# Kernel tuning notes

Measured on AMD Instinct MI355X. Metric: run time of the kernel, lower is better.

The kernel has to match this reference:

```python
import jax, jax.numpy as jnp
import numpy as np

TAU = 0.3
NEG_SLOPE = 0.2
COS_EPS = 1e-8


def _masked_softmax(logits, mask, axis):
    # mask: bool, True = participates. Rows with no True entries yield zeros.
    neg = jnp.finfo(logits.dtype).min
    x = jnp.where(mask, logits, neg)
    x = x - jnp.max(x, axis=axis, keepdims=True)
    e = jnp.exp(x) * mask
    return e / jnp.maximum(jnp.sum(e, axis=axis, keepdims=True), 1e-16)


def _gat_layer(h, adj, W, a_src, a_dst, w_edge, a_edge, b):
    # Dense masked GATConv (heads=1). adj[b,i,j]=True means edge src j -> dst i.
    g = jnp.einsum('bld,dc->blc', h, W)            # projected features
    al_s = jnp.einsum('blc,c->bl', g, a_src)        # per-node src score
    al_d = jnp.einsum('blc,c->bl', g, a_dst)        # per-node dst score
    # edge_attr is constant 1.0 for every thresholded edge, so the edge term
    # lin_edge(1.0) . att_edge collapses to a scalar.
    ae = jnp.dot(w_edge, a_edge)
    logits = jax.nn.leaky_relu(al_d[:, :, None] + al_s[:, None, :] + ae, NEG_SLOPE)
    attn = _masked_softmax(logits, adj, axis=-1)    # softmax over incoming edges per dst
    out = jnp.einsum('bij,bjc->bic', attn, g) + b
    return jax.nn.relu(out)


def setup_inputs() -> dict:
    key = jax.random.key(0)
    B, L, D, H = 16, 1024, 768, 128
    ks = jax.random.split(key, 20)
    inp = {}
    inp['hidden'] = jax.random.normal(ks[0], (B, L, D), jnp.float32)
    inp['attention_mask'] = jax.random.randint(ks[1], (B, L), 0, 2, jnp.int32)

    def lin(k, i, o):
        return jax.random.normal(k, (i, o), jnp.float32) * (1.0 / np.sqrt(i))

    dims = [D, H]
    for l in range(2):
        i = dims[l]
        inp[f'W{l}'] = lin(ks[2 + 6 * l], i, H)
        inp[f'att_src{l}'] = jax.random.normal(ks[3 + 6 * l], (H,), jnp.float32) * 0.1
        inp[f'att_dst{l}'] = jax.random.normal(ks[4 + 6 * l], (H,), jnp.float32) * 0.1
        inp[f'w_edge{l}'] = jax.random.normal(ks[5 + 6 * l], (H,), jnp.float32) * 0.1
        inp[f'att_edge{l}'] = jax.random.normal(ks[6 + 6 * l], (H,), jnp.float32) * 0.1
        inp[f'bias{l}'] = jnp.zeros((H,), jnp.float32)
    out_dim = D + 2 * H            # jk_mode='cat' -> 1024
    hid = max(128, out_dim // 2)   # 512
    inp['S1_W'] = lin(ks[14], out_dim, hid)
    inp['S1_b'] = jnp.zeros((hid,), jnp.float32)
    inp['S2_W'] = lin(ks[15], hid, 1)
    inp['S2_b'] = jnp.zeros((1,), jnp.float32)
    return inp


def reference(hidden, attention_mask,
              W0, att_src0, att_dst0, w_edge0, att_edge0, bias0,
              W1, att_src1, att_dst1, w_edge1, att_edge1, bias1,
              S1_W, S1_b, S2_W, S2_b):
    valid = attention_mask.astype(bool)                         # (B,L)
    # per-batch pairwise cosine similarity graph, thresholded at TAU
    nrm = jnp.linalg.norm(hidden, axis=-1, keepdims=True)
    hn = hidden / jnp.maximum(nrm, COS_EPS)
    sim = jnp.einsum('bld,bmd->blm', hn, hn)                    # (B,L,L)
    adj = (sim > TAU) & valid[:, :, None] & valid[:, None, :]   # bool mask; diag (self loops) kept, sim=1>tau

    h1 = _gat_layer(hidden, adj, W0, att_src0, att_dst0, w_edge0, att_edge0, bias0)
    h2 = _gat_layer(h1, adj, W1, att_src1, att_dst1, w_edge1, att_edge1, bias1)
    h_all = jnp.concatenate([hidden, h1, h2], axis=-1)          # jk 'cat': (B,L,D+2H)

    scores = (jnp.tanh(h_all @ S1_W + S1_b) @ S2_W + S2_b)[..., 0]  # (B,L)
    weights = _masked_softmax(scores, valid, axis=-1)           # segment softmax per batch element
    pooled = jnp.einsum('bl,bld->bd', weights, h_all)           # segment scatter_add pooling
    return pooled
```

## Files before the change

### kernel.cpp

```cpp
#include <hip/hip_runtime.h>

typedef __attribute__((ext_vector_type(8))) short short8;
typedef __attribute__((ext_vector_type(4))) short s4v;
typedef __attribute__((ext_vector_type(4))) float f32x4;
typedef unsigned short u16;
typedef unsigned int u32;
typedef unsigned long long u64;

#define TAU_F 0.3f

__device__ __forceinline__ u16 f2bf(float f){
  u32 u = __float_as_uint(f);
  u32 r = u + 0x7FFFu + ((u >> 16) & 1u);
  return (u16)(r >> 16);
}
__device__ __forceinline__ float bf2f(u16 v){
  return __uint_as_float(((u32)v) << 16);
}
__device__ __forceinline__ float tanh_fast(float x){
  const float e = __expf(2.f * x);
  return 1.f - 2.f / (e + 1.f);
}

typedef __attribute__((address_space(1))) const u32 glb_u32;
typedef __attribute__((address_space(3))) u32 lds_u32;
__device__ __forceinline__ void async_lds16(const void* g, void* l){
  __builtin_amdgcn_global_load_lds((glb_u32*)g, (lds_u32*)l, 16, 0, 0);
}

__global__ __launch_bounds__(1024)
void pre_kernel(float* __restrict__ out, float* __restrict__ scores,
                const float* __restrict__ W0, u16* __restrict__ w0t,
                const float* __restrict__ W1, u16* __restrict__ w1t,
                const float* __restrict__ S1W, u16* __restrict__ s1t,
                const float* __restrict__ wed0, const float* __restrict__ aed0,
                const float* __restrict__ wed1, const float* __restrict__ aed1,
                float* __restrict__ aeb,
                const float* __restrict__ asrc0, const float* __restrict__ adst0,
                const float* __restrict__ asrc1, const float* __restrict__ adst1,
                float* __restrict__ u0, float* __restrict__ v0,
                float* __restrict__ u1, float* __restrict__ v1,
                const int* __restrict__ mask, int* __restrict__ cnt, int* __restrict__ idxb)
{
  __shared__ float lds[64*65];
  const int blk = blockIdx.x, t = threadIdx.x;

  auto tr_tile = [&](const float* in, u16* o, int K, int N, int kt, int ntile) {
    const int r = t >> 4, c0 = (t & 15) * 4;
    const int k0 = kt*64, n0 = ntile*64;
    const float4 v = *(const float4*)&in[(long)(k0 + r)*N + n0 + c0];
    lds[r*65 + c0 + 0] = v.x; lds[r*65 + c0 + 1] = v.y;
    lds[r*65 + c0 + 2] = v.z; lds[r*65 + c0 + 3] = v.w;
    __syncthreads();
    const u64 pk = (u64)f2bf(lds[(c0+0)*65 + r])
                 | ((u64)f2bf(lds[(c0+1)*65 + r]) << 16)
                 | ((u64)f2bf(lds[(c0+2)*65 + r]) << 32)
                 | ((u64)f2bf(lds[(c0+3)*65 + r]) << 48);
    *(u64*)&o[(long)(n0 + r)*K + k0 + c0] = pk;
  };

  if (blk < 16)  { out[blk*1024 + t] = 0.f; return; }
  if (blk < 32)  { scores[(blk-16)*1024 + t] = 0.f; return; }
  if (blk < 56)  { const int id = blk-32;  tr_tile(W0,  w0t, 768, 128, id >> 1, id & 1); return; }
  if (blk < 60)  { const int id = blk-56;  tr_tile(W1,  w1t, 128, 128, id >> 1, id & 1); return; }
  if (blk < 188) { const int id = blk-60;  tr_tile(S1W, s1t, 1024, 512, id >> 3, id & 7); return; }
  if (blk == 188) {
    if (t < 128) { lds[t] = wed0[t]*aed0[t]; lds[128+t] = wed1[t]*aed1[t]; }
    __syncthreads();
    for (int o = 64; o > 0; o >>= 1) { if (t < o) { lds[t] += lds[t+o]; lds[128+t] += lds[128+t+o]; } __syncthreads(); }
    if (t == 0) { aeb[0] = lds[0]; aeb[1] = lds[128]; }
    return;
  }
  if (blk == 189) {
    if (t < 768) {
      float su = 0.f, sv = 0.f;
      for (int c = 0; c < 128; c++) { const float w = W0[t*128 + c]; su += w*asrc0[c]; sv += w*adst0[c]; }
      u0[t] = su; v0[t] = sv;
    }
    return;
  }
  if (blk == 190) {
    if (t < 128) {
      float su = 0.f, sv = 0.f;
      for (int k = 0; k < 128; k++) { const float w = W1[k*128 + t]; su += w*asrc1[k]; sv += w*adst1[k]; }
      u1[t] = su; v1[t] = sv;
    }
    return;
  }
  {
    int* wtot = (int*)lds;
    int* woff = (int*)lds + 16;
    const int b = blk - 191;
    const int w = t >> 6, lane = t & 63;
    const int m = mask[(b << 10) + t];
    const u64 bal = __ballot(m != 0);
    const int pos = __popcll(bal & ((1ull << lane) - 1ull));
    if (lane == 0) wtot[w] = __popcll(bal);
    __syncthreads();
    if (t == 0) { int a = 0; for (int i = 0; i < 16; i++) { woff[i] = a; a += wtot[i]; } cnt[b] = a; }
    __syncthreads();
    if (m) idxb[(b << 10) + woff[w] + pos] = t;
  }
}

__global__ __launch_bounds__(256)
void hn_kernel(const float* __restrict__ hidden, const int* __restrict__ cnt,
               const int* __restrict__ idx,
               const float* __restrict__ u0, const float* __restrict__ v0,
               const float* __restrict__ aeb,
               u16* __restrict__ hallc, float* __restrict__ rnp,
               float* __restrict__ als, float* __restrict__ ald)
{
  const int gr = blockIdx.x * 4 + (threadIdx.x >> 6);
  const int b = gr >> 10, c = gr & 1023;
  const int lane = threadIdx.x & 63;
  if (c >= cnt[b]) return;
  const int l = idx[gr];
  const float* h = hidden + (long)((b << 10) + l) * 768;
  float x[12]; float ss = 0.f, sa = 0.f, sd = 0.f;
#pragma unroll
  for (int k = 0; k < 12; k++) {
    x[k] = h[k*64 + lane];
    ss += x[k]*x[k];
    sa += x[k]*u0[k*64 + lane];
    sd += x[k]*v0[k*64 + lane];
  }
#pragma unroll
  for (int o = 32; o > 0; o >>= 1) {
    ss += __shfl_xor(ss, o, 64);
    sa += __shfl_xor(sa, o, 64);
    sd += __shfl_xor(sd, o, 64);
  }
  const float inv = 1.f / fmaxf(sqrtf(ss), 1e-8f);
  if (lane == 0) { als[gr] = sa; ald[gr] = sd + aeb[0]; rnp[gr] = inv; }
#pragma unroll
  for (int k = 0; k < 12; k++)
    hallc[(long)gr*1024 + k*64 + lane] = f2bf(x[k]);
}

__global__ __launch_bounds__(256)
void mega_kernel(const u16* __restrict__ hallc, const u16* __restrict__ w0t,
                 const u16* __restrict__ s1t, const float* __restrict__ rn,
                 unsigned char* __restrict__ adjp, u16* __restrict__ gtp,
                 u16* __restrict__ partial, const int* __restrict__ cnt)
{
  __shared__ u16 lA[2][64*64];
  __shared__ u16 lB[2][64*64];
  const int t = threadIdx.x, w = t >> 6, lane = t & 63;
  const int bid = blockIdx.x;
  int mode, bz = 0, i0, n0, lda, ldb, ti = 0, tj = 0, cb = 0;
  const u16 *Ab, *Bb;
  if (bid < 2176) {
    mode = 0;
    const int xcd = bid & 7, s = bid >> 3;
    const int hi = (s >= 136) ? 1 : 0;
    bz = xcd*2 + hi;
    int rem = s - hi*136, width = 16;
    while (rem >= width) { rem -= width; ti++; width--; }
    tj = ti + rem;
    i0 = ti*64; n0 = tj*64;
    cb = cnt[bz];
    if (i0 >= cb || n0 >= cb) return;
    Ab = hallc + (((long)bz << 10) << 10);
    Bb = Ab; lda = 1024; ldb = 1024;
  } else if (bid < 2688) {
    mode = 1;
    const int id = bid - 2176;
    i0 = (((id & 7) << 5) + ((id >> 3) & 31)) * 64;
    n0 = (id >> 8) * 64;
    if ((i0 & 1023) >= cnt[i0 >> 10]) return;
    Ab = hallc; lda = 1024; Bb = w0t; ldb = 768;
  } else {
    mode = 2;
    const int id = bid - 2688;
    i0 = (((id & 7) << 5) + ((id >> 3) & 31)) * 64;
    n0 = (id >> 8) * 64;
    if ((i0 & 1023) >= cnt[i0 >> 10]) return;
    Ab = hallc; lda = 1024; Bb = s1t; ldb = 1024;
  }
  const int wr = w >> 1, wc = w & 1;
  const int srow = t >> 3, scg = t & 7;
  const int sc0 = ((scg ^ (srow & 7)) << 3);
  const long arow0 = (long)(i0 + srow) * lda, arow1 = (long)(i0 + srow + 32) * lda;
  const long brow0 = (long)(n0 + srow) * ldb, brow1 = (long)(n0 + srow + 32) * ldb;
  const int rA = lane & 15, kg = lane >> 4;
  const int sw = rA & 7;
  const int off0 = ((kg ^ sw) << 3);
  const int off1 = (((4 + kg) ^ sw) << 3);
  const int rowA0 = (wr*32 + rA) * 64, rowA1 = (wr*32 + 16 + rA) * 64;
  const int rowB0 = (wc*32 + rA) * 64, rowB1 = (wc*32 + 16 + rA) * 64;
  f32x4 acc[2][2] = {};

  auto stage = [&](int buf, int kt) {
    async_lds16(Ab + arow0 + kt + sc0, &lA[buf][t*8]);
    async_lds16(Ab + arow1 + kt + sc0, &lA[buf][2048 + t*8]);
    async_lds16(Bb + brow0 + kt + sc0, &lB[buf][t*8]);
    async_lds16(Bb + brow1 + kt + sc0, &lB[buf][2048 + t*8]);
  };
  auto compute = [&](int buf) {
    short8 a00 = *(const short8*)&lA[buf][rowA0 + off0];
    short8 a01 = *(const short8*)&lA[buf][rowA0 + off1];
    short8 a10 = *(const short8*)&lA[buf][rowA1 + off0];
    short8 a11 = *(const short8*)&lA[buf][rowA1 + off1];
    short8 b00 = *(const short8*)&lB[buf][rowB0 + off0];
    short8 b01 = *(const short8*)&lB[buf][rowB0 + off1];
    short8 b10 = *(const short8*)&lB[buf][rowB1 + off0];
    short8 b11 = *(const short8*)&lB[buf][rowB1 + off1];
    acc[0][0] = __builtin_amdgcn_mfma_f32_16x16x32_bf16(a00, b00, acc[0][0], 0, 0, 0);
    acc[0][1] = __builtin_amdgcn_mfma_f32_16x16x32_bf16(a00, b10, acc[0][1], 0, 0, 0);
    acc[1][0] = __builtin_amdgcn_mfma_f32_16x16x32_bf16(a10, b00, acc[1][0], 0, 0, 0);
    acc[1][1] = __builtin_amdgcn_mfma_f32_16x16x32_bf16(a10, b10, acc[1][1], 0, 0, 0);
    acc[0][0] = __builtin_amdgcn_mfma_f32_16x16x32_bf16(a01, b01, acc[0][0], 0, 0, 0);
    acc[0][1] = __builtin_amdgcn_mfma_f32_16x16x32_bf16(a01, b11, acc[0][1], 0, 0, 0);
    acc[1][0] = __builtin_amdgcn_mfma_f32_16x16x32_bf16(a11, b01, acc[1][0], 0, 0, 0);
    acc[1][1] = __builtin_amdgcn_mfma_f32_16x16x32_bf16(a11, b11, acc[1][1], 0, 0, 0);
  };

  stage(0, 0);
  __syncthreads();
  int cur = 0;
  for (int kt = 1; kt < 12; kt++) {
    stage(cur ^ 1, kt << 6);
    compute(cur);
    __syncthreads();
    cur ^= 1;
  }
  compute(cur);

#pragma unroll
  for (int m = 0; m < 2; m++) {
    const int gi0 = i0 + wr*32 + m*16 + kg*4;
#pragma unroll
    for (int n = 0; n < 2; n++) {
      const int gj = n0 + wc*32 + n*16 + rA;
#pragma unroll
      for (int r = 0; r < 4; r++) {
        const int gi = gi0 + r;
        const float c = acc[m][n][r];
        if (mode == 0) {
          if (gi < cb && gj < cb) {
            const float sim = c * rn[(bz << 10) + gi] * rn[(bz << 10) + gj];
            const unsigned char e = (sim > TAU_F) ? 1 : 0;
            adjp[((long)bz << 20) + ((long)gi << 10) + gj] = e;
            if (ti != tj) adjp[((long)bz << 20) + ((long)gj << 10) + gi] = e;
          }
        } else if (mode == 1) {
          const int b = gi >> 10, l = gi & 1023;
          gtp[(((long)(b*128 + gj)) << 10) + l] = f2bf(c);
        } else {
          partial[(long)gi * 512 + gj] = f2bf(c);
        }
      }
    }
  }
}

__global__ __launch_bounds__(256)
void scorer_fin(const u16* __restrict__ hallc, const u16* __restrict__ s1t,
                const u16* __restrict__ partial, const int* __restrict__ cnt,
                const float* __restrict__ s1b, const float* __restrict__ s2w,
                float* __restrict__ scoresp)
{
  __shared__ u16 lA[2][64*64];
  __shared__ u16 lB[2][64*64];
  __shared__ float sgrid[64];
  const int t = threadIdx.x, w = t >> 6, lane = t & 63;
  const int id = blockIdx.x;
  const int i0 = (((id & 7) << 5) + ((id >> 3) & 31)) * 64;
  const int n0 = (id >> 8) * 64;
  if ((i0 & 1023) >= cnt[i0 >> 10]) return;
  if (t < 64) sgrid[t] = 0.f;
  const int wr = w >> 1, wc = w & 1;
  const int srow = t >> 3, scg = t & 7;
  const int sc0 = ((scg ^ (srow & 7)) << 3);
  const long arow0 = (long)(i0 + srow) * 1024 + 768, arow1 = (long)(i0 + srow + 32) * 1024 + 768;
  const long brow0 = (long)(n0 + srow) * 1024 + 768, brow1 = (long)(n0 + srow + 32) * 1024 + 768;
  const int rA = lane & 15, kg = lane >> 4;
  const int sw = rA & 7;
  const int off0 = ((kg ^ sw) << 3);
  const int off1 = (((4 + kg) ^ sw) << 3);
  const int rowA0 = (wr*32 + rA) * 64, rowA1 = (wr*32 + 16 + rA) * 64;
  const int rowB0 = (wc*32 + rA) * 64, rowB1 = (wc*32 + 16 + rA) * 64;
  f32x4 acc[2][2] = {};

  auto stage = [&](int buf, int kt) {
    async_lds16(hallc + arow0 + kt + sc0, &lA[buf][t*8]);
    async_lds16(hallc + arow1 + kt + sc0, &lA[buf][2048 + t*8]);
    async_lds16(s1t + brow0 + kt + sc0, &lB[buf][t*8]);
    async_lds16(s1t + brow1 + kt + sc0, &lB[buf][2048 + t*8]);
  };
  auto compute = [&](int buf) {
    short8 a00 = *(const short8*)&lA[buf][rowA0 + off0];
    short8 a01 = *(const short8*)&lA[buf][rowA0 + off1];
    short8 a10 = *(const short8*)&lA[buf][rowA1 + off0];
    short8 a11 = *(const short8*)&lA[buf][rowA1 + off1];
    short8 b00 = *(const short8*)&lB[buf][rowB0 + off0];
    short8 b01 = *(const short8*)&lB[buf][rowB0 + off1];
    short8 b10 = *(const short8*)&lB[buf][rowB1 + off0];
    short8 b11 = *(const short8*)&lB[buf][rowB1 + off1];
    acc[0][0] = __builtin_amdgcn_mfma_f32_16x16x32_bf16(a00, b00, acc[0][0], 0, 0, 0);
    acc[0][1] = __builtin_amdgcn_mfma_f32_16x16x32_bf16(a00, b10, acc[0][1], 0, 0, 0);
    acc[1][0] = __builtin_amdgcn_mfma_f32_16x16x32_bf16(a10, b00, acc[1][0], 0, 0, 0);
    acc[1][1] = __builtin_amdgcn_mfma_f32_16x16x32_bf16(a10, b10, acc[1][1], 0, 0, 0);
    acc[0][0] = __builtin_amdgcn_mfma_f32_16x16x32_bf16(a01, b01, acc[0][0], 0, 0, 0);
    acc[0][1] = __builtin_amdgcn_mfma_f32_16x16x32_bf16(a01, b11, acc[0][1], 0, 0, 0);
    acc[1][0] = __builtin_amdgcn_mfma_f32_16x16x32_bf16(a11, b01, acc[1][0], 0, 0, 0);
    acc[1][1] = __builtin_amdgcn_mfma_f32_16x16x32_bf16(a11, b11, acc[1][1], 0, 0, 0);
  };

  stage(0, 0);
  __syncthreads();
  int cur = 0;
  for (int kt = 1; kt < 4; kt++) {
    stage(cur ^ 1, kt << 6);
    compute(cur);
    __syncthreads();
    cur ^= 1;
  }
  compute(cur);

#pragma unroll
  for (int m = 0; m < 2; m++)
#pragma unroll
    for (int r = 0; r < 4; r++) {
      const int gi = i0 + wr*32 + m*16 + kg*4 + r;
      float contrib = 0.f;
#pragma unroll
      for (int n = 0; n < 2; n++) {
        const int gj = n0 + wc*32 + n*16 + rA;
        const float p = acc[m][n][r] + bf2f(partial[(long)gi*512 + gj]) + s1b[gj];
        contrib += tanh_fast(p) * s2w[gj];
      }
#pragma unroll
      for (int off = 1; off < 16; off <<= 1) contrib += __shfl_xor(contrib, off, 64);
      if (rA == 0) atomicAdd(&sgrid[wr*32 + m*16 + kg*4 + r], contrib);
    }
  __syncthreads();
  if (t < 64) {
    const int gi = i0 + t;
    if ((gi & 1023) < cnt[gi >> 10]) atomicAdd(&scoresp[gi], sgrid[t]);
  }
}

template<int FUSE>
__global__ __launch_bounds__(256)
void gat_attn(const unsigned char* __restrict__ adj,
              const float* __restrict__ ald, const float* __restrict__ als,
              const u16* __restrict__ gT, const float* __restrict__ bias,
              const int* __restrict__ cnt,
              u16* __restrict__ hall, int hall_off,
              const float* __restrict__ u1, const float* __restrict__ v1,
              const float* __restrict__ aeb1,
              float* __restrict__ als_o, float* __restrict__ ald_o,
              const u16* __restrict__ w1t, u16* __restrict__ gt2)
{
  __shared__ float red[4][16][132];
  __shared__ float ssumw[4][16];
  __shared__ float alds[FUSE ? 16 : 1][17], aldd[FUSE ? 16 : 1][17];
  __shared__ u16 h1s[FUSE ? 16 : 1][136];
  const int t = threadIdx.x, w = t >> 6, lane = t & 63;
  const int o = blockIdx.x;
  const int xcd = o & 7, s = o >> 3;
  const int bz = xcd*2 + (s >> 6);
  const int i0 = (s & 63) * 16;
  const int cb = cnt[bz];
  if (i0 >= cb) return;
  const int rr = lane & 15, kg = lane >> 4;
  const int r0 = i0 + rr;
  const bool rvalid = r0 < cb;
  const float ald0 = ald[(bz << 10) + r0];
  const unsigned char* arow = adj + ((long)bz << 20) + ((long)r0 << 10);
  const float* als_b = als + (bz << 10);
  const u16* gTb = gT + ((long)bz << 17);
  float s0 = 0.f;
  f32x4 acc[8] = {};
  const int jbase = w * 256 + kg * 8;

  u64 aw[8];
#pragma unroll
  for (int it = 0; it < 8; it++) {
    const int jl = jbase + it*32;
    u64 a = 0;
    if (rvalid && jl < cb) {
      a = *(const u64*)(arow + jl);
      const int rem = cb - jl;
      if (rem < 8) a &= (1ull << (rem * 8)) - 1ull;
    }
    aw[it] = a;
  }

#pragma unroll
  for (int it = 0; it < 8; it++) {
    const u64 a0 = aw[it];
    if (__any(a0 != 0ull)) {
      const int jl = jbase + it*32;
      const float4 f0 = *(const float4*)(als_b + jl);
      const float4 f1 = *(const float4*)(als_b + jl + 4);
      const float sv[8] = {f0.x, f0.y, f0.z, f0.w, f1.x, f1.y, f1.z, f1.w};
      short8 pa;
#pragma unroll
      for (int e = 0; e < 8; e++) {
        float x = ald0 + sv[e];
        x = x > 0.f ? x : 0.2f * x;
        const float p = ((a0 >> (8*e)) & 255ull) ? __expf(x) : 0.f;
        s0 += p;
        pa[e] = (short)f2bf(p);
      }
#pragma unroll
      for (int nf = 0; nf < 8; nf++) {
        const short8 b = *(const short8*)&gTb[(long)(nf*16 + rr) * 1024 + jl];
        acc[nf] = __builtin_amdgcn_mfma_f32_16x16x32_bf16(pa, b, acc[nf], 0, 0, 0);
      }
    }
  }

  s0 += __shfl_xor(s0, 16, 64);
  s0 += __shfl_xor(s0, 32, 64);
  if (lane < 16) ssumw[w][lane] = s0;
#pragma unroll
  for (int nf = 0; nf < 8; nf++)
#pragma unroll
    for (int rg = 0; rg < 4; rg++)
      red[w][kg*4 + rg][nf*16 + rr] = acc[nf][rg];
  __syncthreads();

  const int r = t >> 4, c0 = (t & 15) * 8;
  const float sm = ssumw[0][r] + ssumw[1][r] + ssumw[2][r] + ssumw[3][r];
  const float inv = sm > 0.f ? 1.f / sm : 0.f;
  const long gi = ((long)bz << 10) + i0 + r;
  u16* orow = hall + gi * 1024 + hall_off;
  short8 hv;
  float pa_s = 0.f, pa_d = 0.f;
#pragma unroll
  for (int q = 0; q < 8; q++) {
    const int c = c0 + q;
    float v = (red[0][r][c] + red[1][r][c] + red[2][r][c] + red[3][r][c]) * inv + bias[c];
    v = v > 0.f ? v : 0.f;
    hv[q] = (short)f2bf(v);
    if (FUSE) { pa_s += v * u1[c]; pa_d += v * v1[c]; }
  }
  *(short8*)&orow[c0] = hv;
  if (FUSE) {
    *(short8*)&h1s[r][c0] = hv;
    alds[r][t & 15] = pa_s;
    aldd[r][t & 15] = pa_d;
    __syncthreads();
    if (t < 16) {
      float s2 = 0.f, d2 = 0.f;
#pragma unroll
      for (int j = 0; j < 16; j++) { s2 += alds[t][j]; d2 += aldd[t][j]; }
      als_o[(bz << 10) + i0 + t] = s2;
      ald_o[(bz << 10) + i0 + t] = d2 + aeb1[0];
    }
    f32x4 pacc[2] = {};
    short8 paf[4];
#pragma unroll
    for (int ks = 0; ks < 4; ks++)
      paf[ks] = *(const short8*)&h1s[lane & 15][ks*32 + kg*8];
#pragma unroll
    for (int n = 0; n < 2; n++) {
      const int col = w*32 + n*16 + (lane & 15);
#pragma unroll
      for (int ks = 0; ks < 4; ks++) {
        const short8 pb = *(const short8*)&w1t[col*128 + ks*32 + kg*8];
        pacc[n] = __builtin_amdgcn_mfma_f32_16x16x32_bf16(paf[ks], pb, pacc[n], 0, 0, 0);
      }
    }
#pragma unroll
    for (int n = 0; n < 2; n++) {
      const int gj = w*32 + n*16 + (lane & 15);
#pragma unroll
      for (int rg = 0; rg < 4; rg++)
        gt2[(((long)(bz*128 + gj)) << 10) + i0 + kg*4 + rg] = f2bf(pacc[n][rg]);
    }
  }
}

__global__ __launch_bounds__(256)
void pooled_kernel(const u16* __restrict__ hallc, const float* __restrict__ scores,
                   const int* __restrict__ cnt, float* __restrict__ out)
{
  __shared__ float tot[4];
  const int b = blockIdx.y, l0 = blockIdx.x * 64, t = threadIdx.x;
  const int cb = cnt[b];
  if (l0 >= cb) return;
  float part = 0.f;
#pragma unroll
  for (int q = 0; q < 4; q++) {
    const int l = q*256 + t;
    if (l < cb) part += __expf(scores[(b << 10) + l]);
  }
#pragma unroll
  for (int o = 32; o > 0; o >>= 1) part += __shfl_xor(part, o, 64);
  if ((t & 63) == 0) tot[t >> 6] = part;
  __syncthreads();
  const float inv = 1.f / fmaxf(tot[0] + tot[1] + tot[2] + tot[3], 1e-16f);

  const int lim = min(64, cb - l0);
  float a0 = 0.f, a1 = 0.f, a2 = 0.f, a3 = 0.f;
  for (int l = 0; l < lim; l++) {
    const int gl = (b << 10) + l0 + l;
    const float wv = __expf(scores[gl]) * inv;
    const s4v v = *(const s4v*)&hallc[(long)gl*1024 + t*4];
    a0 += wv * bf2f((u16)v[0]);
    a1 += wv * bf2f((u16)v[1]);
    a2 += wv * bf2f((u16)v[2]);
    a3 += wv * bf2f((u16)v[3]);
  }
  atomicAdd(&out[(b<<10) + t*4 + 0], a0);
  atomicAdd(&out[(b<<10) + t*4 + 1], a1);
  atomicAdd(&out[(b<<10) + t*4 + 2], a2);
  atomicAdd(&out[(b<<10) + t*4 + 3], a3);
}

extern "C" void kernel_launch(void* const* d_in, const int* in_sizes, int n_in,
                              void* d_out, int out_size, void* d_ws, size_t ws_size,
                              hipStream_t stream)
{
  const float* hidden = (const float*)d_in[0];
  const int*   mask   = (const int*)d_in[1];
  const float* W0     = (const float*)d_in[2];
  const float* asrc0  = (const float*)d_in[3];
  const float* adst0  = (const float*)d_in[4];
  const float* wed0   = (const float*)d_in[5];
  const float* aed0   = (const float*)d_in[6];
  const float* bias0  = (const float*)d_in[7];
  const float* W1     = (const float*)d_in[8];
  const float* asrc1  = (const float*)d_in[9];
  const float* adst1  = (const float*)d_in[10];
  const float* wed1   = (const float*)d_in[11];
  const float* aed1   = (const float*)d_in[12];
  const float* bias1  = (const float*)d_in[13];
  const float* S1W    = (const float*)d_in[14];
  const float* S1b    = (const float*)d_in[15];
  const float* S2W    = (const float*)d_in[16];
  float* out = (float*)d_out;

  char* ws = (char*)d_ws;
  u16* hallc   = (u16*)(ws + 0);
  u16* partial = (u16*)(ws + 33554432);
  u16* gt2     = (u16*)(ws + 50331648);
  unsigned char* adj = (unsigned char*)(ws + 58720256);
  u16* gt   = (u16*)(ws + 75497472);
  u16* w0t  = (u16*)(ws + 79691776);
  u16* w1t  = (u16*)(ws + 79888384);
  u16* s1t  = (u16*)(ws + 79921152);
  float* ald = (float*)(ws + 80969728);
  float* als = (float*)(ws + 81035264);
  float* scores = (float*)(ws + 81100800);
  float* als1   = (float*)(ws + 81166336);
  float* ald1   = (float*)(ws + 81231872);
  float* aeb    = (float*)(ws + 81297408);
  int*   cnt    = (int*)(ws + 81297920);
  int*   idxb   = (int*)(ws + 81298432);
  float* u0     = (float*)(ws + 81363968);
  float* v0     = (float*)(ws + 81367040);
  float* u1     = (float*)(ws + 81370112);
  float* v1     = (float*)(ws + 81370624);
  float* rn     = (float*)(ws + 81371136);

  pre_kernel<<<207, 1024, 0, stream>>>(out, scores, W0, w0t, W1, w1t, S1W, s1t,
      wed0, aed0, wed1, aed1, aeb, asrc0, adst0, asrc1, adst1,
      u0, v0, u1, v1, mask, cnt, idxb);

  hn_kernel<<<4096, 256, 0, stream>>>(hidden, cnt, idxb, u0, v0, aeb, hallc, rn, als, ald);

  mega_kernel<<<4736, 256, 0, stream>>>(hallc, w0t, s1t, rn, adj, gt, partial, cnt);

  gat_attn<1><<<1024, 256, 0, stream>>>(adj, ald, als, gt, bias0, cnt, hallc, 768,
        u1, v1, aeb + 1, als1, ald1, w1t, gt2);

  gat_attn<0><<<1024, 256, 0, stream>>>(adj, ald1, als1, gt2, bias1, cnt, hallc, 896,
        nullptr, nullptr, nullptr, nullptr, nullptr, nullptr, nullptr);

  scorer_fin<<<2048, 256, 0, stream>>>(hallc, s1t, partial, cnt, S1b, S2W, scores);

  pooled_kernel<<<dim3(16,16), 256, 0, stream>>>(hallc, scores, cnt, out);
}
```

Before: 115.1 us.

## Parallelize W0 projection precompute, deepen GEMM prefetch, split pooling finer

Three separate changes. The serial u0/v0 precompute, which ran in a single block, is spread over six blocks that use vectorized float4 loads and a shuffle reduction. The mega_kernel GEMM loop now prefetches two stages ahead, waiting on vmcnt counts and raw s_barriers instead of __syncthreads. The pooling kernel uses 16 rows per block instead of 64, giving four times more blocks at the cost of more atomic adds and repeated softmax-sum computation per block.

```diff
diff --git a/kernel.cpp b/kernel.cpp
--- a/kernel.cpp
+++ b/kernel.cpp
@@ -71,15 +71,25 @@
     if (t == 0) { aeb[0] = lds[0]; aeb[1] = lds[128]; }
     return;
   }
-  if (blk == 189) {
-    if (t < 768) {
-      float su = 0.f, sv = 0.f;
-      for (int c = 0; c < 128; c++) { const float w = W0[t*128 + c]; su += w*asrc0[c]; sv += w*adst0[c]; }
-      u0[t] = su; v0[t] = sv;
-    }
+  if (blk < 195) {
+    const int q = blk - 189;
+    const int row = q*128 + (t >> 3);
+    const int c0 = (t & 7) * 16;
+    float su = 0.f, sv = 0.f;
+#pragma unroll
+    for (int i = 0; i < 16; i += 4) {
+      const float4 wv = *(const float4*)&W0[row*128 + c0 + i];
+      const float4 sa = *(const float4*)&asrc0[c0 + i];
+      const float4 da = *(const float4*)&adst0[c0 + i];
+      su += wv.x*sa.x + wv.y*sa.y + wv.z*sa.z + wv.w*sa.w;
+      sv += wv.x*da.x + wv.y*da.y + wv.z*da.z + wv.w*da.w;
+    }
+    su += __shfl_xor(su, 1, 64); su += __shfl_xor(su, 2, 64); su += __shfl_xor(su, 4, 64);
+    sv += __shfl_xor(sv, 1, 64); sv += __shfl_xor(sv, 2, 64); sv += __shfl_xor(sv, 4, 64);
+    if ((t & 7) == 0) { u0[row] = su; v0[row] = sv; }
     return;
   }
-  if (blk == 190) {
+  if (blk == 195) {
     if (t < 128) {
       float su = 0.f, sv = 0.f;
       for (int k = 0; k < 128; k++) { const float w = W1[k*128 + t]; su += w*asrc1[k]; sv += w*adst1[k]; }
@@ -90,7 +100,7 @@
   {
     int* wtot = (int*)lds;
     int* woff = (int*)lds + 16;
-    const int b = blk - 191;
+    const int b = blk - 196;
     const int w = t >> 6, lane = t & 63;
     const int m = mask[(b << 10) + t];
     const u64 bal = __ballot(m != 0);
@@ -217,15 +227,22 @@
   };
 
   stage(0, 0);
-  __syncthreads();
+  stage(1, 64);
   int cur = 0;
-  for (int kt = 1; kt < 12; kt++) {
-    stage(cur ^ 1, kt << 6);
+  for (int kt = 0; kt < 10; kt++) {
+    asm volatile("s_waitcnt vmcnt(4)" ::: "memory");
+    __builtin_amdgcn_s_barrier();
     compute(cur);
-    __syncthreads();
+    __builtin_amdgcn_s_barrier();
+    stage(cur, (kt + 2) << 6);
     cur ^= 1;
   }
+  asm volatile("s_waitcnt vmcnt(4)" ::: "memory");
+  __builtin_amdgcn_s_barrier();
   compute(cur);
+  asm volatile("s_waitcnt vmcnt(0)" ::: "memory");
+  __builtin_amdgcn_s_barrier();
+  compute(cur ^ 1);
 
 #pragma unroll
   for (int m = 0; m < 2; m++) {
@@ -481,7 +498,7 @@
                    const int* __restrict__ cnt, float* __restrict__ out)
 {
   __shared__ float tot[4];
-  const int b = blockIdx.y, l0 = blockIdx.x * 64, t = threadIdx.x;
+  const int b = blockIdx.y, l0 = blockIdx.x * 16, t = threadIdx.x;
   const int cb = cnt[b];
   if (l0 >= cb) return;
   float part = 0.f;
@@ -496,7 +513,7 @@
   __syncthreads();
   const float inv = 1.f / fmaxf(tot[0] + tot[1] + tot[2] + tot[3], 1e-16f);
 
-  const int lim = min(64, cb - l0);
+  const int lim = min(16, cb - l0);
   float a0 = 0.f, a1 = 0.f, a2 = 0.f, a3 = 0.f;
   for (int l = 0; l < lim; l++) {
     const int gl = (b << 10) + l0 + l;
@@ -559,7 +576,7 @@
   float* v1     = (float*)(ws + 81370624);
   float* rn     = (float*)(ws + 81371136);
 
-  pre_kernel<<<207, 1024, 0, stream>>>(out, scores, W0, w0t, W1, w1t, S1W, s1t,
+  pre_kernel<<<212, 1024, 0, stream>>>(out, scores, W0, w0t, W1, w1t, S1W, s1t,
       wed0, aed0, wed1, aed1, aeb, asrc0, adst0, asrc1, adst1,
       u0, v0, u1, v1, mask, cnt, idxb);
 
@@ -575,5 +592,5 @@
 
   scorer_fin<<<2048, 256, 0, stream>>>(hallc, s1t, partial, cnt, S1b, S2W, scores);
 
-  pooled_kernel<<<dim3(16,16), 256, 0, stream>>>(hallc, scores, cnt, out);
-}
+  pooled_kernel<<<dim3(64,16), 256, 0, stream>>>(hallc, scores, cnt, out);
+}
```

Result: faster. 97.79 us (-15.0%).
